# Kernel tuning notes

Hardware: AMD Instinct MI355X
Metric: run time of the kernel (lower is better)

## Reference

```python
import jax, jax.numpy as jnp
import numpy as np

T, N, H, V = 200, 256, 128, 50000

def setup_inputs() -> dict:
    key = jax.random.key(0)
    ks = jax.random.split(key, 8)
    return {
        "sequence_matrix": jax.random.randint(ks[0], (T, N), 0, V),
        "sequence_masks_matrix": jnp.ones((T, N), dtype=jnp.float32),
        "topo_masks": jax.random.uniform(ks[1], (T, N, T), dtype=jnp.float32),
        "W": jax.random.normal(ks[2], (H, 4 * H), dtype=jnp.float32) * 0.05,
        "U": jax.random.normal(ks[3], (H, 4 * H), dtype=jnp.float32) * 0.05,
        "b": jnp.zeros((4 * H,), dtype=jnp.float32),
        "embedding_table": jax.random.normal(ks[4], (V, H), dtype=jnp.float32) * 0.05,
        "W_out": jax.random.normal(ks[5], (H, V), dtype=jnp.float32) * 0.05,
        "b_out": jnp.zeros((V,), dtype=jnp.float32),
    }


def _topolstm_forward(sequence_masks_matrix, topo_masks, W, U, b,
                      embedding_table, W_out, b_out, sequence_matrix):
    emb_seq = embedding_table[sequence_matrix]  # (T, N, H)
    h_init = jnp.zeros((T, N, H), dtype=W.dtype)
    c_init = jnp.zeros((T, N, H), dtype=W.dtype)

    def step(carry, xs):
        h_store, c_store = carry
        t, seq_m, topo_m, emb = xs  # (), (N,), (N,T), (N,H)
        # masked aggregation over prior stored states
        h_sum = jnp.einsum('nt,tnh->nh', topo_m, h_store)
        c_sum = jnp.einsum('nt,tnh->nh', topo_m, c_store)
        gates = h_sum @ U + emb @ W + b  # (N, 4H)
        i, f, o, g = jnp.split(gates, 4, axis=1)
        i, f, o = jax.nn.sigmoid(i), jax.nn.sigmoid(f), jax.nn.sigmoid(o)
        c = seq_m[:, None] * (f * c_sum + i * jnp.tanh(g))
        h = seq_m[:, None] * (o * jnp.tanh(c))
        h_store = jax.lax.dynamic_update_index_in_dim(h_store, h, t, 0)
        c_store = jax.lax.dynamic_update_index_in_dim(c_store, c, t, 0)
        return (h_store, c_store), None

    ts = jnp.arange(T)
    (h_store, _), _ = jax.lax.scan(
        step, (h_init, c_init), (ts, sequence_masks_matrix, topo_masks, emb_seq))

    h_sum = (sequence_masks_matrix[:, :, None] * h_store).sum(axis=0)  # (N, H)
    lengths = sequence_masks_matrix.sum(axis=0)  # (N,)
    h_mean = h_sum / lengths[:, None]
    return h_mean @ W_out + b_out  # (N, V)


def reference(sequence_matrix, sequence_masks_matrix, topo_masks,
              W, U, b, embedding_table, W_out, b_out):
    return _topolstm_forward(sequence_masks_matrix, topo_masks, W, U, b,
                             embedding_table, W_out, b_out, sequence_matrix)
```

## Files before the change

kernel.cpp:

```cpp
#include <hip/hip_runtime.h>
#include <hip/hip_bf16.h>

#define TT 200
#define NBATCH 256
#define HID 128
#define G4 512
#define VOC 50000


#define RL(v, l) __uint_as_float((unsigned)__builtin_amdgcn_readlane((int)__float_as_uint(v), (l)))

#define BAR_LGKM() do { \
    asm volatile("s_waitcnt lgkmcnt(0)" ::: "memory"); \
    __builtin_amdgcn_s_barrier(); \
} while (0)

__global__ __launch_bounds__(512) void kxw(
    const float* __restrict__ ET,
    const float* __restrict__ W,
    const float* __restrict__ b,
    float* __restrict__ XW)
{
    const int tid = threadIdx.x;
    const int jq = tid & 127;
    const int j0 = jq * 4;
    const int rg = tid >> 7;
    const int rb = blockIdx.x * 32;

    __shared__ __align__(16) float et[32][HID];

    {
        const int bse = tid * 8;
        const int r = bse >> 7, c = bse & 127;
        int row = rb + r; row = row < VOC ? row : VOC - 1;
        const float4* src = (const float4*)(ET + (size_t)row * HID + c);
        float4 v0 = src[0], v1 = src[1];
        *((float4*)&et[r][c])     = v0;
        *((float4*)&et[r][c + 4]) = v1;
    }
    __syncthreads();

    float acc[8][4];
    #pragma unroll
    for (int r = 0; r < 8; ++r) {
        acc[r][0] = 0.f; acc[r][1] = 0.f; acc[r][2] = 0.f; acc[r][3] = 0.f;
    }

    const float4* W4 = (const float4*)W;
    #pragma unroll 2
    for (int k4 = 0; k4 < 32; ++k4) {
        const float4 w0 = W4[(size_t)(4 * k4 + 0) * 128 + jq];
        const float4 w1 = W4[(size_t)(4 * k4 + 1) * 128 + jq];
        const float4 w2 = W4[(size_t)(4 * k4 + 2) * 128 + jq];
        const float4 w3 = W4[(size_t)(4 * k4 + 3) * 128 + jq];
        #pragma unroll
        for (int r = 0; r < 8; ++r) {
            const float4 e4 = *(const float4*)&et[rg * 8 + r][4 * k4];
            acc[r][0] = fmaf(e4.x, w0.x, acc[r][0]);
            acc[r][0] = fmaf(e4.y, w1.x, acc[r][0]);
            acc[r][0] = fmaf(e4.z, w2.x, acc[r][0]);
            acc[r][0] = fmaf(e4.w, w3.x, acc[r][0]);
            acc[r][1] = fmaf(e4.x, w0.y, acc[r][1]);
            acc[r][1] = fmaf(e4.y, w1.y, acc[r][1]);
            acc[r][1] = fmaf(e4.z, w2.y, acc[r][1]);
            acc[r][1] = fmaf(e4.w, w3.y, acc[r][1]);
            acc[r][2] = fmaf(e4.x, w0.z, acc[r][2]);
            acc[r][2] = fmaf(e4.y, w1.z, acc[r][2]);
            acc[r][2] = fmaf(e4.z, w2.z, acc[r][2]);
            acc[r][2] = fmaf(e4.w, w3.z, acc[r][2]);
            acc[r][3] = fmaf(e4.x, w0.w, acc[r][3]);
            acc[r][3] = fmaf(e4.y, w1.w, acc[r][3]);
            acc[r][3] = fmaf(e4.z, w2.w, acc[r][3]);
            acc[r][3] = fmaf(e4.w, w3.w, acc[r][3]);
        }
    }

    const float4 bj = *(const float4*)&b[j0];
    #pragma unroll
    for (int r = 0; r < 8; ++r) {
        const int row = rb + rg * 8 + r;
        if (row < VOC) {
            float4 o;
            o.x = acc[r][0] + bj.x; o.y = acc[r][1] + bj.y;
            o.z = acc[r][2] + bj.z; o.w = acc[r][3] + bj.w;
            *(float4*)&XW[(size_t)row * G4 + j0] = o;
        }
    }
}

__global__ __launch_bounds__(1024) void k2_recur(
    const float* __restrict__ topo,
    const float* __restrict__ mask,
    const float* __restrict__ U,
    const int*   __restrict__ seq,
    const float* __restrict__ XW,
    float* __restrict__ hmT)
{
    const int n    = blockIdx.x;
    const int tid  = threadIdx.x;
    const int g    = __builtin_amdgcn_readfirstlane(tid >> 7);
    const int h    = tid & 127;
    const int kh   = __builtin_amdgcn_readfirstlane(tid >> 9);
    const int j    = tid & 511;
    const int lane = tid & 63;

    __shared__ float c_lds[HID][209];
    __shared__ __align__(16) float topoS[2][8][32];
    __shared__ float part_h[8][HID];
    __shared__ float part_c[8][HID];
    __shared__ float pB[2][G4];
    __shared__ float xgl[2][G4];
    __shared__ int   seq_l[TT];
    __shared__ float mask_l[TT];

    float ucol[64];
    #pragma unroll
    for (int kk = 0; kk < 64; ++kk) ucol[kk] = U[(size_t)(kh * 64 + kk) * G4 + j];

    float hreg[25];
    #pragma unroll
    for (int k = 0; k < 25; ++k) hreg[k] = 0.f;
    for (int i = tid; i < HID * 209; i += 1024) (&c_lds[0][0])[i] = 0.f;

    if (tid < TT) {
        seq_l[tid]  = seq[tid * NBATCH + n];
        mask_l[tid] = mask[tid * NBATCH + n];
    }
    if (tid < G4) {
        xgl[0][tid] = XW[(size_t)seq[n] * G4 + tid];
    } else if (tid < 768) {
        const int tt = tid - 512;
        const int gg = tt >> 5, ii = tt & 31;
        topoS[0][gg][ii] = (ii < 25)
            ? topo[(size_t)n * TT + 25 * gg + ii] : 0.f;
    }

    float hmacc = 0.f, len = 0.f;
    __syncthreads();

    for (int t = 0; t < TT; ++t) {
        const int cur = t & 1, nxt = cur ^ 1;
        const int gstar = t / 25;

        const int tn = (t + 1 < TT) ? t + 1 : t;
        float pf = 0.f;
        if (tid < G4) {
            pf = XW[(size_t)seq_l[tn] * G4 + tid];
        } else if (tid < 768) {
            const int tt = tid - 512;
            const int gg = tt >> 5, ii = tt & 31;
            pf = (ii < 25)
                ? topo[((size_t)tn * NBATCH + n) * TT + 25 * gg + ii] : 0.f;
        }
        const float m = mask_l[t];

        const float tval = topoS[cur][g][lane & 31];
        float ah0 = 0.f, ah1 = 0.f, ac0 = 0.f, ac1 = 0.f;
        const int base = 25 * g;
        const float* crow = &c_lds[h][0];
        #pragma unroll
        for (int kk = 0; kk < 6; ++kk) {
            if (base + 4 * kk < t) {
                const float t0 = RL(tval, 4 * kk + 0);
                const float t1 = RL(tval, 4 * kk + 1);
                const float t2 = RL(tval, 4 * kk + 2);
                const float t3 = RL(tval, 4 * kk + 3);
                ah0 = fmaf(t0, hreg[4*kk+0], ah0);
                ac0 = fmaf(t0, crow[base+4*kk+0], ac0);
                ah1 = fmaf(t1, hreg[4*kk+1], ah1);
                ac1 = fmaf(t1, crow[base+4*kk+1], ac1);
                ah0 = fmaf(t2, hreg[4*kk+2], ah0);
                ac0 = fmaf(t2, crow[base+4*kk+2], ac0);
                ah1 = fmaf(t3, hreg[4*kk+3], ah1);
                ac1 = fmaf(t3, crow[base+4*kk+3], ac1);
            }
        }
        if (base + 24 < t) {
            const float tpl = RL(tval, 24);
            ah0 = fmaf(tpl, hreg[24], ah0);
            ac0 = fmaf(tpl, crow[base+24], ac0);
        }
        part_h[g][h] = ah0 + ah1;
        part_c[g][h] = ac0 + ac1;
        BAR_LGKM();

        {
            const int col = kh * 64 + lane;
            const float s0 = part_h[0][col] + part_h[1][col];
            const float s1 = part_h[2][col] + part_h[3][col];
            const float s2 = part_h[4][col] + part_h[5][col];
            const float s3 = part_h[6][col] + part_h[7][col];
            const float hval = (s0 + s1) + (s2 + s3);
            float a0 = 0.f, a1 = 0.f, a2 = 0.f, a3 = 0.f;
            #pragma unroll
            for (int q = 0; q < 16; ++q) {
                a0 = fmaf(RL(hval, 4*q+0), ucol[4*q+0], a0);
                a1 = fmaf(RL(hval, 4*q+1), ucol[4*q+1], a1);
                a2 = fmaf(RL(hval, 4*q+2), ucol[4*q+2], a2);
                a3 = fmaf(RL(hval, 4*q+3), ucol[4*q+3], a3);
            }
            pB[kh][j] = (a0 + a1) + (a2 + a3);
        }
        float csr = 0.f;
        if (g == gstar) {
            const float c0 = part_c[0][h] + part_c[1][h];
            const float c1 = part_c[2][h] + part_c[3][h];
            const float c2 = part_c[4][h] + part_c[5][h];
            const float c3 = part_c[6][h] + part_c[7][h];
            csr = (c0 + c1) + (c2 + c3);
        }
        if (tid < G4) {
            xgl[nxt][tid] = pf;
        } else if (tid < 768) {
            const int tt = tid - 512;
            topoS[nxt][tt >> 5][tt & 31] = pf;
        }
        BAR_LGKM();

        if (g == gstar) {
            const float iv = pB[0][h]       + pB[1][h]       + xgl[cur][h];
            const float fv = pB[0][128+h]   + pB[1][128+h]   + xgl[cur][128+h];
            const float ov = pB[0][256+h]   + pB[1][256+h]   + xgl[cur][256+h];
            const float gv = pB[0][384+h]   + pB[1][384+h]   + xgl[cur][384+h];
            const float si = 1.f / (1.f + expf(-iv));
            const float sf = 1.f / (1.f + expf(-fv));
            const float so = 1.f / (1.f + expf(-ov));
            const float tg = tanhf(gv);
            const float cn = m * (sf * csr + si * tg);
            const float hn = m * (so * tanhf(cn));
            const int kt = t - 25 * gstar;
            #pragma unroll
            for (int k = 0; k < 25; ++k) if (k == kt) hreg[k] = hn;
            c_lds[h][t] = cn;
            hmacc = fmaf(m, hn, hmacc);
        }
        len += m;
    }

    part_h[g][h] = hmacc;
    __syncthreads();
    if (tid < HID) {
        float s = 0.f;
        #pragma unroll
        for (int gg = 0; gg < 8; ++gg) s += part_h[gg][tid];
        hmT[(size_t)tid * NBATCH + n] = s / len;
    }
}

__global__ __launch_bounds__(512) void k3_out(
    const float* __restrict__ hmT,
    const float* __restrict__ Wout,
    const float* __restrict__ bout,
    float* __restrict__ out)
{
    const int tid = threadIdx.x;
    const int v = blockIdx.x * 512 + tid;
    const int r0 = blockIdx.y * 32;
    const int vc = v < VOC ? v : VOC - 1;

    float acc[32];
    #pragma unroll
    for (int r = 0; r < 32; ++r) acc[r] = 0.f;

    #pragma unroll 2
    for (int k = 0; k < HID; ++k) {
        const float wv = Wout[(size_t)k * VOC + vc];
        const float* hr = hmT + k * NBATCH + r0;
        #pragma unroll
        for (int r = 0; r < 32; ++r) acc[r] = fmaf(hr[r], wv, acc[r]);
    }
    const float bv = bout[vc];
    if (v < VOC) {
        for (int r = 0; r < 32; ++r)
            out[(size_t)(r0 + r) * VOC + v] = acc[r] + bv;
    }
}

extern "C" void kernel_launch(void* const* d_in, const int* in_sizes, int n_in,
                              void* d_out, int out_size, void* d_ws, size_t ws_size,
                              hipStream_t stream) {
    const int*   seq  = (const int*)d_in[0];
    const float* msk  = (const float*)d_in[1];
    const float* topo = (const float*)d_in[2];
    const float* W    = (const float*)d_in[3];
    const float* U    = (const float*)d_in[4];
    const float* b    = (const float*)d_in[5];
    const float* ET   = (const float*)d_in[6];
    const float* Wout = (const float*)d_in[7];
    const float* bout = (const float*)d_in[8];
    float* out = (float*)d_out;

    float* XW  = (float*)d_ws;
    float* hmT = (float*)((char*)d_ws + (size_t)VOC * G4 * sizeof(float));

    kxw<<<(VOC + 31) / 32, 512, 0, stream>>>(ET, W, b, XW);
    k2_recur<<<NBATCH, 1024, 0, stream>>>(topo, msk, U, seq, XW, hmT);
    k3_out<<<dim3(98, 8), 512, 0, stream>>>(hmT, Wout, bout, out);
}
```

Baseline: 747.6 us.

## Interleave time steps across groups in recurrence and vectorize output GEMM

The recurrent kernel now assigns time step t to group t&7 (round-robin) instead of contiguous blocks of 25, so the work of the masked aggregation over prior states is spread evenly across the 8 groups rather than concentrated in the lowest groups. The topo mask load and c_lds indexing are remapped to match the strided layout. Separately, the output projection kernel processes 4 vocab columns per thread with float4 loads and stores and 16 rows per block, increasing memory access width and per-thread reuse of hmT. The strided c_lds accesses may change LDS bank behaviour.

```diff
diff --git a/kernel.cpp b/kernel.cpp
--- a/kernel.cpp
+++ b/kernel.cpp
@@ -132,7 +132,7 @@
         const int tt = tid - 512;
         const int gg = tt >> 5, ii = tt & 31;
         topoS[0][gg][ii] = (ii < 25)
-            ? topo[(size_t)n * TT + 25 * gg + ii] : 0.f;
+            ? topo[(size_t)n * TT + gg + 8 * ii] : 0.f;
     }
 
     float hmacc = 0.f, len = 0.f;
@@ -140,7 +140,8 @@
 
     for (int t = 0; t < TT; ++t) {
         const int cur = t & 1, nxt = cur ^ 1;
-        const int gstar = t / 25;
+        const int gstar = t & 7;
+        const int kt = t >> 3;
 
         const int tn = (t + 1 < TT) ? t + 1 : t;
         float pf = 0.f;
@@ -150,35 +151,34 @@
             const int tt = tid - 512;
             const int gg = tt >> 5, ii = tt & 31;
             pf = (ii < 25)
-                ? topo[((size_t)tn * NBATCH + n) * TT + 25 * gg + ii] : 0.f;
+                ? topo[((size_t)tn * NBATCH + n) * TT + gg + 8 * ii] : 0.f;
         }
         const float m = mask_l[t];
 
         const float tval = topoS[cur][g][lane & 31];
         float ah0 = 0.f, ah1 = 0.f, ac0 = 0.f, ac1 = 0.f;
-        const int base = 25 * g;
         const float* crow = &c_lds[h][0];
         #pragma unroll
         for (int kk = 0; kk < 6; ++kk) {
-            if (base + 4 * kk < t) {
+            if (g + 32 * kk < t) {
                 const float t0 = RL(tval, 4 * kk + 0);
                 const float t1 = RL(tval, 4 * kk + 1);
                 const float t2 = RL(tval, 4 * kk + 2);
                 const float t3 = RL(tval, 4 * kk + 3);
                 ah0 = fmaf(t0, hreg[4*kk+0], ah0);
-                ac0 = fmaf(t0, crow[base+4*kk+0], ac0);
+                ac0 = fmaf(t0, crow[g + 32*kk +  0], ac0);
                 ah1 = fmaf(t1, hreg[4*kk+1], ah1);
-                ac1 = fmaf(t1, crow[base+4*kk+1], ac1);
+                ac1 = fmaf(t1, crow[g + 32*kk +  8], ac1);
                 ah0 = fmaf(t2, hreg[4*kk+2], ah0);
-                ac0 = fmaf(t2, crow[base+4*kk+2], ac0);
+                ac0 = fmaf(t2, crow[g + 32*kk + 16], ac0);
                 ah1 = fmaf(t3, hreg[4*kk+3], ah1);
-                ac1 = fmaf(t3, crow[base+4*kk+3], ac1);
+                ac1 = fmaf(t3, crow[g + 32*kk + 24], ac1);
             }
         }
-        if (base + 24 < t) {
+        if (g + 192 < t) {
             const float tpl = RL(tval, 24);
             ah0 = fmaf(tpl, hreg[24], ah0);
-            ac0 = fmaf(tpl, crow[base+24], ac0);
+            ac0 = fmaf(tpl, crow[g + 192], ac0);
         }
         part_h[g][h] = ah0 + ah1;
         part_c[g][h] = ac0 + ac1;
@@ -228,7 +228,6 @@
             const float tg = tanhf(gv);
             const float cn = m * (sf * csr + si * tg);
             const float hn = m * (so * tanhf(cn));
-            const int kt = t - 25 * gstar;
             #pragma unroll
             for (int k = 0; k < 25; ++k) if (k == kt) hreg[k] = hn;
             c_lds[h][t] = cn;
@@ -254,25 +253,38 @@
     float* __restrict__ out)
 {
     const int tid = threadIdx.x;
-    const int v = blockIdx.x * 512 + tid;
-    const int r0 = blockIdx.y * 32;
-    const int vc = v < VOC ? v : VOC - 1;
-
-    float acc[32];
-    #pragma unroll
-    for (int r = 0; r < 32; ++r) acc[r] = 0.f;
+    const int v0 = blockIdx.x * 2048 + tid * 4;
+    const int r0 = blockIdx.y * 16;
+    const int vc = v0 < VOC ? v0 : VOC - 4;
+
+    float acc[16][4];
+    #pragma unroll
+    for (int r = 0; r < 16; ++r) {
+        acc[r][0] = 0.f; acc[r][1] = 0.f; acc[r][2] = 0.f; acc[r][3] = 0.f;
+    }
 
     #pragma unroll 2
     for (int k = 0; k < HID; ++k) {
-        const float wv = Wout[(size_t)k * VOC + vc];
+        const float4 wv = *(const float4*)&Wout[(size_t)k * VOC + vc];
         const float* hr = hmT + k * NBATCH + r0;
         #pragma unroll
-        for (int r = 0; r < 32; ++r) acc[r] = fmaf(hr[r], wv, acc[r]);
-    }
-    const float bv = bout[vc];
-    if (v < VOC) {
-        for (int r = 0; r < 32; ++r)
-            out[(size_t)(r0 + r) * VOC + v] = acc[r] + bv;
+        for (int r = 0; r < 16; ++r) {
+            const float hv = hr[r];
+            acc[r][0] = fmaf(hv, wv.x, acc[r][0]);
+            acc[r][1] = fmaf(hv, wv.y, acc[r][1]);
+            acc[r][2] = fmaf(hv, wv.z, acc[r][2]);
+            acc[r][3] = fmaf(hv, wv.w, acc[r][3]);
+        }
+    }
+    if (v0 < VOC) {
+        const float4 bv = *(const float4*)&bout[v0];
+        #pragma unroll
+        for (int r = 0; r < 16; ++r) {
+            float4 o;
+            o.x = acc[r][0] + bv.x; o.y = acc[r][1] + bv.y;
+            o.z = acc[r][2] + bv.z; o.w = acc[r][3] + bv.w;
+            *(float4*)&out[(size_t)(r0 + r) * VOC + v0] = o;
+        }
     }
 }
 
@@ -295,5 +307,5 @@
 
     kxw<<<(VOC + 31) / 32, 512, 0, stream>>>(ET, W, b, XW);
     k2_recur<<<NBATCH, 1024, 0, stream>>>(topo, msk, U, seq, XW, hmT);
-    k3_out<<<dim3(98, 8), 512, 0, stream>>>(hmT, Wout, bout, out);
+    k3_out<<<dim3(25, 16), 512, 0, stream>>>(hmT, Wout, bout, out);
 }
```

After: 726.8 us. -2.8%, faster.
